# Optimization experiments

Hardware: AMD Instinct MI355X
Metric: run time of the kernel (lower is better)

Reference implementation:

```python
import jax, jax.numpy as jnp
import numpy as np

B, C, W, H = 8192, 512, 14, 4
D = C // H  # head dim = 128


def setup_inputs() -> dict:
    key = jax.random.key(0)
    ks = jax.random.split(key, 8)
    s = 1.0 / np.sqrt(C).astype(np.float32)
    return {
        "x": jax.random.normal(ks[0], (B, C, W), jnp.float32),
        "Wq": jax.random.normal(ks[1], (C, C), jnp.float32) * s,
        "bq": jax.random.normal(ks[2], (C,), jnp.float32) * 0.01,
        "Wk": jax.random.normal(ks[3], (C, C), jnp.float32) * s,
        "bk": jax.random.normal(ks[4], (C,), jnp.float32) * 0.01,
        "Wv": jax.random.normal(ks[5], (C, C), jnp.float32) * s,
        "bv": jax.random.normal(ks[6], (C,), jnp.float32) * 0.01,
        "rel_w": jax.random.normal(ks[7], (1, H, D, W), jnp.float32),
    }


def reference(x, Wq, bq, Wk, bk, Wv, bv, rel_w):
    # Conv1d(kernel_size=1) == channel-wise linear: out[b,o,w] = sum_c Wm[o,c]*x[b,c,w] + bm[o]
    def proj(Wm, bm):
        y = jnp.einsum('oc,bcw->bow', Wm, x) + bm[None, :, None]
        return y.reshape(B, H, D, W)

    q = proj(Wq, bq)  # [B,H,D,W]
    k = proj(Wk, bk)
    v = proj(Wv, bv)

    # content-content: q^T k over head dim -> [B,H,W,W]
    cc = jnp.einsum('bhdi,bhdj->bhij', q, k)
    # content-position: rel_w^T q -> [B,H,W,W] (rows = relative position, cols = query pos)
    cp = jnp.einsum('hdi,bhdj->bhij', rel_w[0], q)

    attn = jax.nn.softmax(cc + cp, axis=-1)  # softmax over last dim, as in the original

    # out = v @ attn^T : out[b,h,d,i] = sum_j v[b,h,d,j] * attn[b,h,i,j]
    out = jnp.einsum('bhdj,bhij->bhdi', v, attn)
    return out.reshape(B, C, W)
```

## Files before the change

### kernel.cpp

```cpp
#include <hip/hip_runtime.h>
#include <hip/hip_bf16.h>

typedef __bf16 bf16x8 __attribute__((ext_vector_type(8)));
typedef float f32x4 __attribute__((ext_vector_type(4)));
typedef int i32x4 __attribute__((ext_vector_type(4)));

typedef __attribute__((address_space(1))) const void GVoid;
typedef __attribute__((address_space(3))) void LVoid;

#define SX1 16.0f
#define SX1I 0.0625f
#define SX2 4000.0f
#define SW1 400.0f
#define SW1I 0.0025f
#define SW2 100000.0f
#define SR1 32.0f
#define SR1I 0.03125f
#define SR2 8000.0f
#define SC_QK 1.5625e-4f
#define SC_CP 1.953125e-3f
#define CORR 0.004f

static __device__ __forceinline__ float b2f(unsigned short u) {
    union { float f; unsigned int i; } x; x.i = ((unsigned int)u) << 16; return x.f;
}
static __device__ __forceinline__ unsigned short f2b(float f) {
    union { float f; unsigned int u; } x; x.f = f;
    unsigned int r = x.u + 0x7FFFu + ((x.u >> 16) & 1u);
    return (unsigned short)(r >> 16);
}
static __device__ __forceinline__ int q8(float v, float s) {
    int i = __float2int_rn(v * s);
    return (i > 127) ? 127 : (i < -127 ? -127 : i);
}

__global__ __launch_bounds__(256) void k_prep(const float* __restrict__ Wq, const float* __restrict__ Wk,
                                              const float* __restrict__ Wv, const float* __restrict__ bq,
                                              const float* __restrict__ bk, const float* __restrict__ bv,
                                              const float* __restrict__ relw, char* __restrict__ Wi8,
                                              unsigned short* __restrict__ Wvh, float* __restrict__ biasA,
                                              float* __restrict__ biasV) {
    int o = blockIdx.x;
    int tid = threadIdx.x;
    if (o < 1024) {
        const float* src = (o < 512) ? (Wq + (long)o * 512) : (Wk + (long)(o - 512) * 512);
        char* row = Wi8 + (long)o * 1024;
        for (int c = tid; c < 512; c += 256) {
            float w = src[c];
            int wh = q8(w, SW1);
            float res = w - (float)wh * SW1I;
            int wl = q8(res, SW2);
            row[c] = (char)wh;
            row[512 + c] = (char)wl;
        }
    } else if (o < 1536) {
        const float* src = Wv + (long)(o - 1024) * 512;
        for (int c = tid; c < 512; c += 256) Wvh[(long)(o - 1024) * 512 + c] = f2b(src[c]);
    } else if (o < 1592) {
        int t = o - 1536, h = t / 14, i = t - h * 14;
        char* row = Wi8 + (long)(1024 + t) * 1024;
#pragma unroll
        for (int cc = 0; cc < 2; ++cc) {
            int c = tid + cc * 256;
            float acc = 0.f;
            for (int d = 0; d < 128; ++d)
                acc += relw[h * 1792 + d * 14 + i] * Wq[(long)(h * 128 + d) * 512 + c];
            int rh = q8(acc, SR1);
            float res = acc - (float)rh * SR1I;
            int rl = q8(res, SR2);
            row[c] = (char)rh;
            row[512 + c] = (char)rl;
        }
        if (tid == 0) {
            float acc = 0.f;
            for (int d = 0; d < 128; ++d) acc += relw[h * 1792 + d * 14 + i] * bq[h * 128 + d];
            biasA[1024 + t] = acc;
        }
    } else {
        for (int i = tid; i < 1152; i += 256) {
            if (i >= 1024 && i < 1080) continue;
            biasA[i] = (i < 512) ? bq[i] : (i < 1024) ? bk[i - 512] : 0.f;
        }
        for (int i = tid; i < 512; i += 256) biasV[i] = bv[i];
        int* z = (int*)(Wi8 + 1080 * 1024);
        for (int idx = tid; idx < 72 * 256; idx += 256) z[idx] = 0;
    }
}

__global__ __launch_bounds__(256) void k_transpose(const float* __restrict__ x,
                                                   char* __restrict__ Ai8,
                                                   unsigned short* __restrict__ Ah16, int b0) {
    __shared__ float xl[512 * 15];
    const float* xb = x + (long)(b0 + blockIdx.x) * 7168;
    const float4* xb4 = (const float4*)xb;
    int tid = threadIdx.x;
#pragma unroll
    for (int it = 0; it < 7; ++it) {
        int f = tid + it * 256;
        float4 v = xb4[f];
        float vals[4] = {v.x, v.y, v.z, v.w};
        int e = f * 4;
#pragma unroll
        for (int j = 0; j < 4; ++j) {
            int ee = e + j;
            int c = (ee * 9363) >> 17;
            int w = ee - c * 14;
            xl[c * 15 + w] = vals[j];
        }
    }
    __syncthreads();
    char* irow = Ai8 + (long)blockIdx.x * 14336;
    unsigned short* hrow = Ah16 + (long)blockIdx.x * 7168;
#pragma unroll
    for (int it = 0; it < 7; ++it) {
        int p = tid + it * 256;
        int w = p >> 7, c0 = (p & 127) * 4;
        unsigned int hp = 0, lp = 0;
        unsigned short hb[4];
#pragma unroll
        for (int j = 0; j < 4; ++j) {
            float v = xl[(c0 + j) * 15 + w];
            int xh = q8(v, SX1);
            float res = v - (float)xh * SX1I;
            int xlo = q8(res, SX2);
            hp |= ((unsigned int)(xh & 255)) << (8 * j);
            lp |= ((unsigned int)(xlo & 255)) << (8 * j);
            hb[j] = f2b(v);
        }
        *(unsigned int*)(irow + (long)w * 1024 + c0) = hp;
        *(unsigned int*)(irow + (long)w * 1024 + 512 + c0) = lp;
        *(unsigned long long*)(hrow + (long)w * 512 + c0) =
            (unsigned long long)hb[0] | ((unsigned long long)hb[1] << 16) |
            ((unsigned long long)hb[2] << 32) | ((unsigned long long)hb[3] << 48);
    }
}

__global__ __launch_bounds__(256) void k_gemmA(const char* __restrict__ Ai8,
                                               const char* __restrict__ Wi8,
                                               const float* __restrict__ biasA,
                                               float* __restrict__ qkf, int Mtiles) {
    __shared__ char Ahs[128 * 64];
    __shared__ char Als[128 * 64];
    __shared__ char Bhs[128 * 64];
    __shared__ char Bls[128 * 64];
    int nwg = Mtiles * 9;
    int p = blockIdx.x;
    int xcd = p & 7, o8 = p >> 3;
    int q8_ = nwg >> 3, r8 = nwg & 7;
    int t = (xcd < r8 ? xcd * (q8_ + 1) : r8 * (q8_ + 1) + (xcd - r8) * q8_) + o8;
    int mt = t / 9, nt = t - mt * 9;
    long m0 = (long)mt * 128;
    int n0 = nt * 128;
    int tid = threadIdx.x, lane = tid & 63, wv = tid >> 6;
    int wr = wv >> 1, wc = wv & 1;
    int rrow = lane >> 2;
    int u = lane & 3;

    i32x4 accM[4][4], accC[4][4];
#pragma unroll
    for (int i = 0; i < 4; ++i)
#pragma unroll
        for (int j = 0; j < 4; ++j) { accM[i][j] = (i32x4){0, 0, 0, 0}; accC[i][j] = (i32x4){0, 0, 0, 0}; }

    for (int kt = 0; kt < 8; ++kt) {
        int kof = kt * 64;
#pragma unroll
        for (int ci = 0; ci < 2; ++ci) {
            int ch = wv * 2 + ci;
            int row = ch * 16 + rrow;
            int gu = ((u ^ (row & 3)) << 4);
            const char* sa = Ai8 + ((m0 + row) << 10) + kof + gu;
            const char* sb = Wi8 + ((long)(n0 + row) << 10) + kof + gu;
            __builtin_amdgcn_global_load_lds((GVoid*)sa, (LVoid*)(Ahs + ch * 1024), 16, 0, 0);
            __builtin_amdgcn_global_load_lds((GVoid*)(sa + 512), (LVoid*)(Als + ch * 1024), 16, 0, 0);
            __builtin_amdgcn_global_load_lds((GVoid*)sb, (LVoid*)(Bhs + ch * 1024), 16, 0, 0);
            __builtin_amdgcn_global_load_lds((GVoid*)(sb + 512), (LVoid*)(Bls + ch * 1024), 16, 0, 0);
        }
        asm volatile("s_waitcnt vmcnt(0)" ::: "memory");
        __syncthreads();

        i32x4 ah[4], al[4], bh[4], bl[4];
#pragma unroll
        for (int mf = 0; mf < 4; ++mf) {
            int row = wr * 64 + mf * 16 + (lane & 15);
            int off = row * 64 + (((lane >> 4) ^ (row & 3)) << 4);
            ah[mf] = *(const i32x4*)(Ahs + off);
            al[mf] = *(const i32x4*)(Als + off);
        }
#pragma unroll
        for (int nf = 0; nf < 4; ++nf) {
            int row = wc * 64 + nf * 16 + (lane & 15);
            int off = row * 64 + (((lane >> 4) ^ (row & 3)) << 4);
            bh[nf] = *(const i32x4*)(Bhs + off);
            bl[nf] = *(const i32x4*)(Bls + off);
        }
#pragma unroll
        for (int mf = 0; mf < 4; ++mf)
#pragma unroll
            for (int nf = 0; nf < 4; ++nf) {
                accM[mf][nf] = __builtin_amdgcn_mfma_i32_16x16x64_i8(ah[mf], bh[nf], accM[mf][nf], 0, 0, 0);
                accC[mf][nf] = __builtin_amdgcn_mfma_i32_16x16x64_i8(ah[mf], bl[nf], accC[mf][nf], 0, 0, 0);
                accC[mf][nf] = __builtin_amdgcn_mfma_i32_16x16x64_i8(al[mf], bh[nf], accC[mf][nf], 0, 0, 0);
            }
        __syncthreads();
    }
#pragma unroll
    for (int nf = 0; nf < 4; ++nf) {
        int n = n0 + wc * 64 + nf * 16 + (lane & 15);
        float scale = (n < 1024) ? SC_QK : SC_CP;
        float bb = biasA[n];
#pragma unroll
        for (int mf = 0; mf < 4; ++mf) {
            long mg = m0 + wr * 64 + mf * 16 + ((lane >> 4) << 2);
#pragma unroll
            for (int r = 0; r < 4; ++r) {
                float val = ((float)accM[mf][nf][r] + CORR * (float)accC[mf][nf][r]) * scale + bb;
                if (n < 1080) qkf[(mg + r) * 1152 + n] = val;
            }
        }
    }
}

__global__ __launch_bounds__(256) void k_gemmv(const unsigned short* __restrict__ Ah16,
                                               const unsigned short* __restrict__ Wvh,
                                               const float* __restrict__ biasV,
                                               unsigned short* __restrict__ vb, int Mtiles) {
    __shared__ unsigned short Ash[128 * 64];
    __shared__ unsigned short Bsh[128 * 64];
    int nwg = Mtiles * 4;
    int p = blockIdx.x;
    int xcd = p & 7, o8 = p >> 3;
    int q8_ = nwg >> 3, r8 = nwg & 7;
    int t = (xcd < r8 ? xcd * (q8_ + 1) : r8 * (q8_ + 1) + (xcd - r8) * q8_) + o8;
    int mt = t >> 2, nt = t & 3;
    long m0 = (long)mt * 128;
    int n0 = nt * 128;
    int tid = threadIdx.x, lane = tid & 63, wv = tid >> 6;
    int wr = wv >> 1, wc = wv & 1;
    int rrow = lane >> 3;
    int u = lane & 7;

    f32x4 acc[4][4];
#pragma unroll
    for (int i = 0; i < 4; ++i)
#pragma unroll
        for (int j = 0; j < 4; ++j) acc[i][j] = (f32x4){0.f, 0.f, 0.f, 0.f};

    for (int kt = 0; kt < 8; ++kt) {
        int kofs = kt * 64;
#pragma unroll
        for (int ti = 0; ti < 4; ++ti) {
            int chunk = wv * 4 + ti;
            int row = chunk * 8 + rrow;
            int colel = ((u ^ (row & 7)) << 3);
            const unsigned short* sa = Ah16 + ((m0 + row) << 9) + kofs + colel;
            const unsigned short* sb = Wvh + ((long)(n0 + row) << 9) + kofs + colel;
            __builtin_amdgcn_global_load_lds((GVoid*)sa, (LVoid*)(Ash + chunk * 512), 16, 0, 0);
            __builtin_amdgcn_global_load_lds((GVoid*)sb, (LVoid*)(Bsh + chunk * 512), 16, 0, 0);
        }
        asm volatile("s_waitcnt vmcnt(0)" ::: "memory");
        __syncthreads();
#pragma unroll
        for (int kk = 0; kk < 2; ++kk) {
            bf16x8 af[4], bfr[4];
            int kb = kk * 64 + ((lane >> 4) << 4);
#pragma unroll
            for (int mf = 0; mf < 4; ++mf) {
                int row = wr * 64 + mf * 16 + (lane & 15);
                af[mf] = *(const bf16x8*)((const char*)Ash + row * 128 + (kb ^ ((row & 7) << 4)));
            }
#pragma unroll
            for (int nf = 0; nf < 4; ++nf) {
                int row = wc * 64 + nf * 16 + (lane & 15);
                bfr[nf] = *(const bf16x8*)((const char*)Bsh + row * 128 + (kb ^ ((row & 7) << 4)));
            }
#pragma unroll
            for (int mf = 0; mf < 4; ++mf)
#pragma unroll
                for (int nf = 0; nf < 4; ++nf)
                    acc[mf][nf] = __builtin_amdgcn_mfma_f32_16x16x32_bf16(af[mf], bfr[nf], acc[mf][nf], 0, 0, 0);
        }
        __syncthreads();
    }
#pragma unroll
    for (int nf = 0; nf < 4; ++nf) {
        int n = n0 + wc * 64 + nf * 16 + (lane & 15);
        float bb = biasV[n];
#pragma unroll
        for (int mf = 0; mf < 4; ++mf) {
            long mg = m0 + wr * 64 + mf * 16 + ((lane >> 4) << 2);
#pragma unroll
            for (int r = 0; r < 4; ++r)
                vb[(mg + r) * 512 + n] = f2b(acc[mf][nf][r] + bb);
        }
    }
}

__global__ __launch_bounds__(512) void k_attn(const float* __restrict__ qkf,
                                              const unsigned short* __restrict__ vb,
                                              float* __restrict__ out, int b0) {
    __shared__ float qs[14 * 512];
    __shared__ float ks[14 * 512];
    __shared__ float cps[56 * 16];
    __shared__ float sl[56 * 16];
    __shared__ unsigned short vs[14 * 512];
    int tid = threadIdx.x;
    long mb = (long)blockIdx.x * 14;
    const float4* qk4 = (const float4*)qkf;
#pragma unroll
    for (int it = 0; it < 7; ++it) {
        int idx = tid + it * 512;
        int w = idx >> 8, c4 = idx & 255;
        float4 v = qk4[(mb + w) * 288 + c4];
        if (c4 < 128) *(float4*)&qs[w * 512 + ((c4 ^ (w & 7)) << 2)] = v;
        else {
            int uu = c4 - 128;
            *(float4*)&ks[w * 512 + ((uu ^ (w & 7)) << 2)] = v;
        }
    }
#pragma unroll
    for (int it = 0; it < 2; ++it) {
        int idx = tid + it * 512;
        if (idx < 784) {
            int w = idx / 56, tt = idx - w * 56;
            cps[tt * 16 + w] = qkf[(mb + w) * 1152 + 1024 + tt];
        }
    }
#pragma unroll
    for (int it = 0; it < 2; ++it) {
        int idx = tid + it * 512;
        if (idx < 896) {
            int w = idx >> 6, uu = idx & 63;
            *(uint4*)&vs[w * 512 + uu * 8] = *(const uint4*)&vb[(mb + w) * 512 + uu * 8];
        }
    }
    __syncthreads();
    if (tid < 196) {
        int h = tid / 49, r = tid - h * 49;
        int i0 = (r / 7) * 2, j0 = (r - (r / 7) * 7) * 2;
        float a00 = 0.f, a01 = 0.f, a10 = 0.f, a11 = 0.f;
#pragma unroll
        for (int d4 = 0; d4 < 32; ++d4) {
            int uu = h * 32 + d4;
            float4 qa = *(const float4*)&qs[i0 * 512 + ((uu ^ (i0 & 7)) << 2)];
            float4 qb = *(const float4*)&qs[(i0 + 1) * 512 + ((uu ^ ((i0 + 1) & 7)) << 2)];
            float4 ka = *(const float4*)&ks[j0 * 512 + ((uu ^ (j0 & 7)) << 2)];
            float4 kb = *(const float4*)&ks[(j0 + 1) * 512 + ((uu ^ ((j0 + 1) & 7)) << 2)];
            a00 += qa.x * ka.x + qa.y * ka.y + qa.z * ka.z + qa.w * ka.w;
            a01 += qa.x * kb.x + qa.y * kb.y + qa.z * kb.z + qa.w * kb.w;
            a10 += qb.x * ka.x + qb.y * ka.y + qb.z * ka.z + qb.w * ka.w;
            a11 += qb.x * kb.x + qb.y * kb.y + qb.z * kb.z + qb.w * kb.w;
        }
        int base = (h * 14 + i0) * 16 + j0;
        sl[base] = a00 + cps[base];
        sl[base + 1] = a01 + cps[base + 1];
        sl[base + 16] = a10 + cps[base + 16];
        sl[base + 17] = a11 + cps[base + 17];
    }
    __syncthreads();
    if (tid < 56) {
        float* row = &sl[tid * 16];
        float m = row[0];
#pragma unroll
        for (int j = 1; j < 14; ++j) m = fmaxf(m, row[j]);
        float ex[14]; float sum = 0.f;
#pragma unroll
        for (int j = 0; j < 14; ++j) { ex[j] = __expf(row[j] - m); sum += ex[j]; }
        float inv = 1.f / sum;
#pragma unroll
        for (int j = 0; j < 14; ++j) row[j] = ex[j] * inv;
    }
    __syncthreads();
    int c = tid, h = c >> 7;
    float vr[14];
#pragma unroll
    for (int j = 0; j < 14; ++j) vr[j] = b2f(vs[j * 512 + c]);
    float* orow = out + (((long)(b0 + blockIdx.x) * 512 + c) * 14);
    float ob[14];
#pragma unroll
    for (int i = 0; i < 14; ++i) {
        const float* ar = &sl[(h * 14 + i) * 16];
        float a = 0.f;
#pragma unroll
        for (int j = 0; j < 14; ++j) a += vr[j] * ar[j];
        ob[i] = a;
    }
#pragma unroll
    for (int t2 = 0; t2 < 7; ++t2)
        *(float2*)(orow + t2 * 2) = make_float2(ob[2 * t2], ob[2 * t2 + 1]);
}

extern "C" void kernel_launch(void* const* d_in, const int* in_sizes, int n_in,
                              void* d_out, int out_size, void* d_ws, size_t ws_size,
                              hipStream_t stream) {
    const float* x    = (const float*)d_in[0];
    const float* Wq   = (const float*)d_in[1];
    const float* bq   = (const float*)d_in[2];
    const float* Wk   = (const float*)d_in[3];
    const float* bk   = (const float*)d_in[4];
    const float* Wv   = (const float*)d_in[5];
    const float* bv   = (const float*)d_in[6];
    const float* relw = (const float*)d_in[7];
    float* out = (float*)d_out;
    char* ws = (char*)d_ws;

    char*           Wi8   = ws;
    unsigned short* Wvh   = (unsigned short*)(ws + 1179648);
    float*          biasA = (float*)(ws + 1703936);
    float*          biasV = (float*)(ws + 1708544);
    const long WS_DATA = 1712640;

    long avail = (long)ws_size - WS_DATA;
    long nbmax = avail / 107520;
    long NBc = (nbmax / 128) * 128;
    if (NBc > 8192) NBc = 8192;
    if (NBc < 128) NBc = 128;

    char*           Ai8  = ws + WS_DATA;
    unsigned short* Ah16 = (unsigned short*)(Ai8 + NBc * 14336);
    float*          qkf  = (float*)(Ah16 + NBc * 7168);
    unsigned short* vbw  = (unsigned short*)(qkf + NBc * 16128);

    k_prep<<<1593, 256, 0, stream>>>(Wq, Wk, Wv, bq, bk, bv, relw, Wi8, Wvh, biasA, biasV);

    for (int b0 = 0; b0 < 8192; b0 += (int)NBc) {
        int nb = 8192 - b0; if (nb > NBc) nb = (int)NBc;
        int Mtiles = (nb * 14) / 128;
        k_transpose<<<nb, 256, 0, stream>>>(x, Ai8, Ah16, b0);
        k_gemmA<<<Mtiles * 9, 256, 0, stream>>>(Ai8, Wi8, biasA, qkf, Mtiles);
        k_gemmv<<<Mtiles * 4, 256, 0, stream>>>(Ah16, Wvh, biasV, vbw, Mtiles);
        k_attn<<<nb, 512, 0, stream>>>(qkf, vbw, out, b0);
    }
}
```

Before: 757.7 us.

## Fuse V projection into int8 split GEMM and drop bf16 activation copy

The V projection moves from a separate bf16 MFMA GEMM into the int8 hi/lo split GEMM. Wv is quantized into extra Wi8 rows and the grid grows from 9 to 13 N-tiles, so one kernel emits q/k/cp floats and bf16 V. This removes the bf16 x copy and its writes, one kernel launch and re-reading the activations. The K tile is widened to 128 with an 8-way swizzle, and V tiles skip the weight-low correction term. V precision now depends on the int8 two-term approximation, which drops the ah×bl term, instead of bf16.

```diff
diff --git a/kernel.cpp b/kernel.cpp
--- a/kernel.cpp
+++ b/kernel.cpp
@@ -29,7 +29,7 @@
     unsigned int r = x.u + 0x7FFFu + ((x.u >> 16) & 1u);
     return (unsigned short)(r >> 16);
 }
-static __device__ __forceinline__ int q8(float v, float s) {
+static __device__ __forceinline__ int q8v(float v, float s) {
     int i = __float2int_rn(v * s);
     return (i > 127) ? 127 : (i < -127 ? -127 : i);
 }
@@ -38,8 +38,7 @@
                                               const float* __restrict__ Wv, const float* __restrict__ bq,
                                               const float* __restrict__ bk, const float* __restrict__ bv,
                                               const float* __restrict__ relw, char* __restrict__ Wi8,
-                                              unsigned short* __restrict__ Wvh, float* __restrict__ biasA,
-                                              float* __restrict__ biasV) {
+                                              float* __restrict__ biasA) {
     int o = blockIdx.x;
     int tid = threadIdx.x;
     if (o < 1024) {
@@ -47,15 +46,23 @@
         char* row = Wi8 + (long)o * 1024;
         for (int c = tid; c < 512; c += 256) {
             float w = src[c];
-            int wh = q8(w, SW1);
+            int wh = q8v(w, SW1);
             float res = w - (float)wh * SW1I;
-            int wl = q8(res, SW2);
+            int wl = q8v(res, SW2);
             row[c] = (char)wh;
             row[512 + c] = (char)wl;
         }
     } else if (o < 1536) {
         const float* src = Wv + (long)(o - 1024) * 512;
-        for (int c = tid; c < 512; c += 256) Wvh[(long)(o - 1024) * 512 + c] = f2b(src[c]);
+        char* row = Wi8 + (long)(1152 + (o - 1024)) * 1024;
+        for (int c = tid; c < 512; c += 256) {
+            float w = src[c];
+            int wh = q8v(w, SW1);
+            float res = w - (float)wh * SW1I;
+            int wl = q8v(res, SW2);
+            row[c] = (char)wh;
+            row[512 + c] = (char)wl;
+        }
     } else if (o < 1592) {
         int t = o - 1536, h = t / 14, i = t - h * 14;
         char* row = Wi8 + (long)(1024 + t) * 1024;
@@ -65,9 +72,9 @@
             float acc = 0.f;
             for (int d = 0; d < 128; ++d)
                 acc += relw[h * 1792 + d * 14 + i] * Wq[(long)(h * 128 + d) * 512 + c];
-            int rh = q8(acc, SR1);
+            int rh = q8v(acc, SR1);
             float res = acc - (float)rh * SR1I;
-            int rl = q8(res, SR2);
+            int rl = q8v(res, SR2);
             row[c] = (char)rh;
             row[512 + c] = (char)rl;
         }
@@ -77,19 +84,17 @@
             biasA[1024 + t] = acc;
         }
     } else {
-        for (int i = tid; i < 1152; i += 256) {
+        for (int i = tid; i < 1664; i += 256) {
             if (i >= 1024 && i < 1080) continue;
-            biasA[i] = (i < 512) ? bq[i] : (i < 1024) ? bk[i - 512] : 0.f;
-        }
-        for (int i = tid; i < 512; i += 256) biasV[i] = bv[i];
-        int* z = (int*)(Wi8 + 1080 * 1024);
+            biasA[i] = (i < 512) ? bq[i] : (i < 1024) ? bk[i - 512] : (i < 1152) ? 0.f : bv[i - 1152];
+        }
+        int* z = (int*)(Wi8 + (long)1080 * 1024);
         for (int idx = tid; idx < 72 * 256; idx += 256) z[idx] = 0;
     }
 }
 
 __global__ __launch_bounds__(256) void k_transpose(const float* __restrict__ x,
-                                                   char* __restrict__ Ai8,
-                                                   unsigned short* __restrict__ Ah16, int b0) {
+                                                   char* __restrict__ Ai8, int b0) {
     __shared__ float xl[512 * 15];
     const float* xb = x + (long)(b0 + blockIdx.x) * 7168;
     const float4* xb4 = (const float4*)xb;
@@ -110,188 +115,115 @@
     }
     __syncthreads();
     char* irow = Ai8 + (long)blockIdx.x * 14336;
-    unsigned short* hrow = Ah16 + (long)blockIdx.x * 7168;
 #pragma unroll
     for (int it = 0; it < 7; ++it) {
         int p = tid + it * 256;
         int w = p >> 7, c0 = (p & 127) * 4;
         unsigned int hp = 0, lp = 0;
-        unsigned short hb[4];
 #pragma unroll
         for (int j = 0; j < 4; ++j) {
             float v = xl[(c0 + j) * 15 + w];
-            int xh = q8(v, SX1);
+            int xh = q8v(v, SX1);
             float res = v - (float)xh * SX1I;
-            int xlo = q8(res, SX2);
+            int xlo = q8v(res, SX2);
             hp |= ((unsigned int)(xh & 255)) << (8 * j);
             lp |= ((unsigned int)(xlo & 255)) << (8 * j);
-            hb[j] = f2b(v);
         }
         *(unsigned int*)(irow + (long)w * 1024 + c0) = hp;
         *(unsigned int*)(irow + (long)w * 1024 + 512 + c0) = lp;
-        *(unsigned long long*)(hrow + (long)w * 512 + c0) =
-            (unsigned long long)hb[0] | ((unsigned long long)hb[1] << 16) |
-            ((unsigned long long)hb[2] << 32) | ((unsigned long long)hb[3] << 48);
     }
 }
 
 __global__ __launch_bounds__(256) void k_gemmA(const char* __restrict__ Ai8,
                                                const char* __restrict__ Wi8,
                                                const float* __restrict__ biasA,
-                                               float* __restrict__ qkf, int Mtiles) {
-    __shared__ char Ahs[128 * 64];
-    __shared__ char Als[128 * 64];
-    __shared__ char Bhs[128 * 64];
-    __shared__ char Bls[128 * 64];
-    int nwg = Mtiles * 9;
+                                               float* __restrict__ qkf,
+                                               unsigned short* __restrict__ vb, int Mtiles) {
+    __shared__ __align__(16) char Ahs[128 * 128];
+    __shared__ __align__(16) char Als[128 * 128];
+    __shared__ __align__(16) char Bhs[128 * 128];
+    __shared__ __align__(16) char Bls[128 * 128];
+    int nwg = Mtiles * 13;
     int p = blockIdx.x;
     int xcd = p & 7, o8 = p >> 3;
     int q8_ = nwg >> 3, r8 = nwg & 7;
     int t = (xcd < r8 ? xcd * (q8_ + 1) : r8 * (q8_ + 1) + (xcd - r8) * q8_) + o8;
-    int mt = t / 9, nt = t - mt * 9;
+    int mt = t / 13, nt = t - mt * 13;
     long m0 = (long)mt * 128;
     int n0 = nt * 128;
-    int tid = threadIdx.x, lane = tid & 63, wv = tid >> 6;
-    int wr = wv >> 1, wc = wv & 1;
-    int rrow = lane >> 2;
-    int u = lane & 3;
-
-    i32x4 accM[4][4], accC[4][4];
-#pragma unroll
-    for (int i = 0; i < 4; ++i)
-#pragma unroll
-        for (int j = 0; j < 4; ++j) { accM[i][j] = (i32x4){0, 0, 0, 0}; accC[i][j] = (i32x4){0, 0, 0, 0}; }
-
-    for (int kt = 0; kt < 8; ++kt) {
-        int kof = kt * 64;
-#pragma unroll
-        for (int ci = 0; ci < 2; ++ci) {
-            int ch = wv * 2 + ci;
-            int row = ch * 16 + rrow;
-            int gu = ((u ^ (row & 3)) << 4);
-            const char* sa = Ai8 + ((m0 + row) << 10) + kof + gu;
-            const char* sb = Wi8 + ((long)(n0 + row) << 10) + kof + gu;
-            __builtin_amdgcn_global_load_lds((GVoid*)sa, (LVoid*)(Ahs + ch * 1024), 16, 0, 0);
-            __builtin_amdgcn_global_load_lds((GVoid*)(sa + 512), (LVoid*)(Als + ch * 1024), 16, 0, 0);
-            __builtin_amdgcn_global_load_lds((GVoid*)sb, (LVoid*)(Bhs + ch * 1024), 16, 0, 0);
-            __builtin_amdgcn_global_load_lds((GVoid*)(sb + 512), (LVoid*)(Bls + ch * 1024), 16, 0, 0);
-        }
-        asm volatile("s_waitcnt vmcnt(0)" ::: "memory");
-        __syncthreads();
-
-        i32x4 ah[4], al[4], bh[4], bl[4];
-#pragma unroll
-        for (int mf = 0; mf < 4; ++mf) {
-            int row = wr * 64 + mf * 16 + (lane & 15);
-            int off = row * 64 + (((lane >> 4) ^ (row & 3)) << 4);
-            ah[mf] = *(const i32x4*)(Ahs + off);
-            al[mf] = *(const i32x4*)(Als + off);
-        }
-#pragma unroll
-        for (int nf = 0; nf < 4; ++nf) {
-            int row = wc * 64 + nf * 16 + (lane & 15);
-            int off = row * 64 + (((lane >> 4) ^ (row & 3)) << 4);
-            bh[nf] = *(const i32x4*)(Bhs + off);
-            bl[nf] = *(const i32x4*)(Bls + off);
-        }
-#pragma unroll
-        for (int mf = 0; mf < 4; ++mf)
-#pragma unroll
-            for (int nf = 0; nf < 4; ++nf) {
-                accM[mf][nf] = __builtin_amdgcn_mfma_i32_16x16x64_i8(ah[mf], bh[nf], accM[mf][nf], 0, 0, 0);
-                accC[mf][nf] = __builtin_amdgcn_mfma_i32_16x16x64_i8(ah[mf], bl[nf], accC[mf][nf], 0, 0, 0);
-                accC[mf][nf] = __builtin_amdgcn_mfma_i32_16x16x64_i8(al[mf], bh[nf], accC[mf][nf], 0, 0, 0);
-            }
-        __syncthreads();
-    }
-#pragma unroll
-    for (int nf = 0; nf < 4; ++nf) {
-        int n = n0 + wc * 64 + nf * 16 + (lane & 15);
-        float scale = (n < 1024) ? SC_QK : SC_CP;
-        float bb = biasA[n];
-#pragma unroll
-        for (int mf = 0; mf < 4; ++mf) {
-            long mg = m0 + wr * 64 + mf * 16 + ((lane >> 4) << 2);
-#pragma unroll
-            for (int r = 0; r < 4; ++r) {
-                float val = ((float)accM[mf][nf][r] + CORR * (float)accC[mf][nf][r]) * scale + bb;
-                if (n < 1080) qkf[(mg + r) * 1152 + n] = val;
-            }
-        }
-    }
-}
-
-__global__ __launch_bounds__(256) void k_gemmv(const unsigned short* __restrict__ Ah16,
-                                               const unsigned short* __restrict__ Wvh,
-                                               const float* __restrict__ biasV,
-                                               unsigned short* __restrict__ vb, int Mtiles) {
-    __shared__ unsigned short Ash[128 * 64];
-    __shared__ unsigned short Bsh[128 * 64];
-    int nwg = Mtiles * 4;
-    int p = blockIdx.x;
-    int xcd = p & 7, o8 = p >> 3;
-    int q8_ = nwg >> 3, r8 = nwg & 7;
-    int t = (xcd < r8 ? xcd * (q8_ + 1) : r8 * (q8_ + 1) + (xcd - r8) * q8_) + o8;
-    int mt = t >> 2, nt = t & 3;
-    long m0 = (long)mt * 128;
-    int n0 = nt * 128;
+    bool isv = (nt >= 9);
     int tid = threadIdx.x, lane = tid & 63, wv = tid >> 6;
     int wr = wv >> 1, wc = wv & 1;
     int rrow = lane >> 3;
     int u = lane & 7;
 
-    f32x4 acc[4][4];
+    i32x4 accM[4][4], accC[4][4];
 #pragma unroll
     for (int i = 0; i < 4; ++i)
 #pragma unroll
-        for (int j = 0; j < 4; ++j) acc[i][j] = (f32x4){0.f, 0.f, 0.f, 0.f};
-
-    for (int kt = 0; kt < 8; ++kt) {
-        int kofs = kt * 64;
+        for (int j = 0; j < 4; ++j) { accM[i][j] = (i32x4){0, 0, 0, 0}; accC[i][j] = (i32x4){0, 0, 0, 0}; }
+
+    for (int kt = 0; kt < 4; ++kt) {
+        int kof = kt * 128;
 #pragma unroll
         for (int ti = 0; ti < 4; ++ti) {
             int chunk = wv * 4 + ti;
             int row = chunk * 8 + rrow;
-            int colel = ((u ^ (row & 7)) << 3);
-            const unsigned short* sa = Ah16 + ((m0 + row) << 9) + kofs + colel;
-            const unsigned short* sb = Wvh + ((long)(n0 + row) << 9) + kofs + colel;
-            __builtin_amdgcn_global_load_lds((GVoid*)sa, (LVoid*)(Ash + chunk * 512), 16, 0, 0);
-            __builtin_amdgcn_global_load_lds((GVoid*)sb, (LVoid*)(Bsh + chunk * 512), 16, 0, 0);
+            int gu = ((u ^ (row & 7)) << 4);
+            const char* sa = Ai8 + ((m0 + row) << 10) + kof + gu;
+            const char* sb = Wi8 + ((long)(n0 + row) << 10) + kof + gu;
+            __builtin_amdgcn_global_load_lds((GVoid*)sa, (LVoid*)(Ahs + chunk * 1024), 16, 0, 0);
+            __builtin_amdgcn_global_load_lds((GVoid*)(sa + 512), (LVoid*)(Als + chunk * 1024), 16, 0, 0);
+            __builtin_amdgcn_global_load_lds((GVoid*)sb, (LVoid*)(Bhs + chunk * 1024), 16, 0, 0);
+            if (!isv)
+                __builtin_amdgcn_global_load_lds((GVoid*)(sb + 512), (LVoid*)(Bls + chunk * 1024), 16, 0, 0);
         }
         asm volatile("s_waitcnt vmcnt(0)" ::: "memory");
         __syncthreads();
 #pragma unroll
         for (int kk = 0; kk < 2; ++kk) {
-            bf16x8 af[4], bfr[4];
+            i32x4 ah[4], al[4], bh[4], bl[4];
             int kb = kk * 64 + ((lane >> 4) << 4);
 #pragma unroll
             for (int mf = 0; mf < 4; ++mf) {
                 int row = wr * 64 + mf * 16 + (lane & 15);
-                af[mf] = *(const bf16x8*)((const char*)Ash + row * 128 + (kb ^ ((row & 7) << 4)));
+                int off = row * 128 + (kb ^ ((row & 7) << 4));
+                ah[mf] = *(const i32x4*)(Ahs + off);
+                al[mf] = *(const i32x4*)(Als + off);
             }
 #pragma unroll
             for (int nf = 0; nf < 4; ++nf) {
                 int row = wc * 64 + nf * 16 + (lane & 15);
-                bfr[nf] = *(const bf16x8*)((const char*)Bsh + row * 128 + (kb ^ ((row & 7) << 4)));
+                int off = row * 128 + (kb ^ ((row & 7) << 4));
+                bh[nf] = *(const i32x4*)(Bhs + off);
+                bl[nf] = *(const i32x4*)(Bls + off);
             }
 #pragma unroll
             for (int mf = 0; mf < 4; ++mf)
 #pragma unroll
-                for (int nf = 0; nf < 4; ++nf)
-                    acc[mf][nf] = __builtin_amdgcn_mfma_f32_16x16x32_bf16(af[mf], bfr[nf], acc[mf][nf], 0, 0, 0);
+                for (int nf = 0; nf < 4; ++nf) {
+                    accM[mf][nf] = __builtin_amdgcn_mfma_i32_16x16x64_i8(ah[mf], bh[nf], accM[mf][nf], 0, 0, 0);
+                    if (!isv)
+                        accC[mf][nf] = __builtin_amdgcn_mfma_i32_16x16x64_i8(ah[mf], bl[nf], accC[mf][nf], 0, 0, 0);
+                    accC[mf][nf] = __builtin_amdgcn_mfma_i32_16x16x64_i8(al[mf], bh[nf], accC[mf][nf], 0, 0, 0);
+                }
         }
         __syncthreads();
     }
 #pragma unroll
     for (int nf = 0; nf < 4; ++nf) {
         int n = n0 + wc * 64 + nf * 16 + (lane & 15);
-        float bb = biasV[n];
+        float scale = (n < 1024) ? SC_QK : (n < 1152 ? SC_CP : SC_QK);
+        float bb = biasA[n];
 #pragma unroll
         for (int mf = 0; mf < 4; ++mf) {
             long mg = m0 + wr * 64 + mf * 16 + ((lane >> 4) << 2);
 #pragma unroll
-            for (int r = 0; r < 4; ++r)
-                vb[(mg + r) * 512 + n] = f2b(acc[mf][nf][r] + bb);
+            for (int r = 0; r < 4; ++r) {
+                float val = ((float)accM[mf][nf][r] + CORR * (float)accC[mf][nf][r]) * scale + bb;
+                if (n < 1080) qkf[(mg + r) * 1152 + n] = val;
+                else if (n >= 1152) vb[(mg + r) * 512 + (n - 1152)] = f2b(val);
+            }
         }
     }
 }
@@ -404,31 +336,27 @@
     float* out = (float*)d_out;
     char* ws = (char*)d_ws;
 
-    char*           Wi8   = ws;
-    unsigned short* Wvh   = (unsigned short*)(ws + 1179648);
-    float*          biasA = (float*)(ws + 1703936);
-    float*          biasV = (float*)(ws + 1708544);
-    const long WS_DATA = 1712640;
+    char*  Wi8   = ws;
+    float* biasA = (float*)(ws + 1703936);
+    const long WS_DATA = 1712128;
 
     long avail = (long)ws_size - WS_DATA;
-    long nbmax = avail / 107520;
+    long nbmax = avail / 93184;
     long NBc = (nbmax / 128) * 128;
     if (NBc > 8192) NBc = 8192;
     if (NBc < 128) NBc = 128;
 
-    char*           Ai8  = ws + WS_DATA;
-    unsigned short* Ah16 = (unsigned short*)(Ai8 + NBc * 14336);
-    float*          qkf  = (float*)(Ah16 + NBc * 7168);
-    unsigned short* vbw  = (unsigned short*)(qkf + NBc * 16128);
-
-    k_prep<<<1593, 256, 0, stream>>>(Wq, Wk, Wv, bq, bk, bv, relw, Wi8, Wvh, biasA, biasV);
+    char*           Ai8 = ws + WS_DATA;
+    float*          qkf = (float*)(Ai8 + NBc * 14336);
+    unsigned short* vbw = (unsigned short*)(qkf + NBc * 16128);
+
+    k_prep<<<1593, 256, 0, stream>>>(Wq, Wk, Wv, bq, bk, bv, relw, Wi8, biasA);
 
     for (int b0 = 0; b0 < 8192; b0 += (int)NBc) {
         int nb = 8192 - b0; if (nb > NBc) nb = (int)NBc;
         int Mtiles = (nb * 14) / 128;
-        k_transpose<<<nb, 256, 0, stream>>>(x, Ai8, Ah16, b0);
-        k_gemmA<<<Mtiles * 9, 256, 0, stream>>>(Ai8, Wi8, biasA, qkf, Mtiles);
-        k_gemmv<<<Mtiles * 4, 256, 0, stream>>>(Ah16, Wvh, biasV, vbw, Mtiles);
+        k_transpose<<<nb, 256, 0, stream>>>(x, Ai8, b0);
+        k_gemmA<<<Mtiles * 13, 256, 0, stream>>>(Ai8, Wi8, biasA, qkf, vbw, Mtiles);
         k_attn<<<nb, 512, 0, stream>>>(qkf, vbw, out, b0);
     }
 }
```

New measurement: 869.1 us. 1.15x slower.
